# Optimization experiments

Measured on AMD Instinct MI355X. Metric: run time of the kernel, lower is better.

The kernel has to match this reference:

```python
import jax, jax.numpy as jnp
import numpy as np
from jax.scipy.linalg import expm

LATENT, HIDDEN, N_PARTS, K = 128, 2048, 128, 2048
OMEGA_DIM, TRANZ_DIM = 9 * N_PARTS, 3 * N_PARTS


def setup_inputs() -> dict:
    key = jax.random.key(0)
    ks = jax.random.split(key, 10)

    def w(k, out_d, in_d):
        # eqx.nn.Linear-style scale ~ 1/sqrt(fan_in)
        return jax.random.normal(k, (out_d, in_d), dtype=jnp.float32) / np.sqrt(in_d)

    return {
        "x_init": jax.random.normal(ks[0], (LATENT, K), dtype=jnp.float32),
        "Wo0": w(ks[1], HIDDEN, LATENT),
        "Wo1": w(ks[2], HIDDEN, HIDDEN),
        "Wo2": w(ks[3], HIDDEN, HIDDEN),
        "Wo3": w(ks[4], OMEGA_DIM, HIDDEN),
        "Wt0": w(ks[5], HIDDEN, LATENT),
        "Wt1": w(ks[6], HIDDEN, HIDDEN),
        "Wt2": w(ks[7], HIDDEN, HIDDEN),
        "Wt3": w(ks[8], TRANZ_DIM, HIDDEN),
    }


def _mlp(weights, x):
    # bias-free MLP, relu on all but last layer; x is (d_in, K)
    for i, W in enumerate(weights):
        x = W @ x
        if i + 1 < len(weights):
            x = jax.nn.relu(x)
    return x


def reference(x_init, Wo0, Wo1, Wo2, Wo3, Wt0, Wt1, Wt2, Wt3):
    omega = _mlp([Wo0, Wo1, Wo2, Wo3], x_init)            # (9n, K)
    n = omega.shape[0] // 9
    k = omega.shape[1]
    # exp_omega 2D branch: vmap over columns, each column -> (n,3,3) expm batch
    mats = omega.T.reshape(k * n, 3, 3)
    R = jax.vmap(expm)(mats).reshape(k, 9 * n)            # (K, 9n)
    rotations = R.T                                        # (9n, K)
    translations = _mlp([Wt0, Wt1, Wt2, Wt3], x_init)     # (3n, K)
    # form_transformations (2D branch): stack translation as a 4th row -> (12n, K)
    rot_r = rotations.reshape(n, 3, 3, k)
    tr_r = translations.reshape(n, 1, 3, k)
    transf = jnp.concatenate([rot_r, tr_r], axis=1).reshape(-1, k)  # (12n, K)
    return (omega, transf, rotations, translations)
```

## Files before the change

kernel.cpp:

```cpp
#include <hip/hip_runtime.h>
#include <stdint.h>


typedef short bf16x8 __attribute__((ext_vector_type(8)));
typedef float f32x4 __attribute__((ext_vector_type(4)));

__device__ __forceinline__ unsigned short f2bf(float f) {
  unsigned int x = __float_as_uint(f);
  unsigned int r = (x + 0x7fffu + ((x >> 16) & 1u)) >> 16;
  return (unsigned short)r;
}

__device__ __forceinline__ void gld_lds16(const void* g, void* l) {
  __builtin_amdgcn_global_load_lds(
      (__attribute__((address_space(1))) void*)(g),
      (__attribute__((address_space(3))) void*)(l),
      16, 0, 0);
}

__global__ void cast_weights_k(const float* __restrict__ wo0, const float* __restrict__ wo1,
                               const float* __restrict__ wo2, const float* __restrict__ wo3,
                               const float* __restrict__ wt0, const float* __restrict__ wt1,
                               const float* __restrict__ wt2, const float* __restrict__ wt3,
                               unsigned short* __restrict__ dst) {
  int gid = blockIdx.x * 256 + threadIdx.x;
  int idx = gid * 4;
  if (idx >= 20447232) return;
  const float* src;
  int off;
  if (idx < 8650752) {
    if (idx < 262144)       { src = wo0; off = idx; }
    else if (idx < 4456448) { src = wo1; off = idx - 262144; }
    else                    { src = wo2; off = idx - 4456448; }
  } else {
    if (idx < 11010048)      { src = wo3; off = idx - 8650752; }
    else if (idx < 11272192) { src = wt0; off = idx - 11010048; }
    else if (idx < 15466496) { src = wt1; off = idx - 11272192; }
    else if (idx < 19660800) { src = wt2; off = idx - 15466496; }
    else                     { src = wt3; off = idx - 19660800; }
  }
  float4 v = *(const float4*)(src + off);
  ushort4 o;
  o.x = f2bf(v.x); o.y = f2bf(v.y); o.z = f2bf(v.z); o.w = f2bf(v.w);
  *(ushort4*)(dst + idx) = o;
}

__global__ void transpose_cast_k(const float* __restrict__ x, unsigned short* __restrict__ xt) {
  __shared__ float tile[32][33];
  const int bx = blockIdx.x, by = blockIdx.y;
  const int tx = threadIdx.x, ty = threadIdx.y;
#pragma unroll
  for (int i = 0; i < 32; i += 8)
    tile[ty + i][tx] = x[(size_t)(by * 32 + ty + i) * 2048 + bx * 32 + tx];
  __syncthreads();
#pragma unroll
  for (int i = 0; i < 32; i += 8)
    xt[(size_t)(bx * 32 + ty + i) * 128 + by * 32 + tx] = f2bf(tile[tx][ty + i]);
}

template <int MODE, int TM, int SWZ>
__global__ __launch_bounds__(256, 2) void gemm_tn(
    const unsigned short* __restrict__ A0, const unsigned short* __restrict__ B0,
    void* __restrict__ C0v, int n0tiles, int ldc0, long csplit0,
    const unsigned short* __restrict__ A1, const unsigned short* __restrict__ B1,
    void* __restrict__ C1v, int ldc1, long csplit1, int Kfull, int Klen) {
  __shared__ unsigned short Asl[TM * 64];
  __shared__ unsigned short Bsl[128 * 64];
  constexpr int TMW = TM / 32;

  int mt, yt;
  if (SWZ) {
    int id = blockIdx.x;
    int xcd = id & 7, s = id >> 3;
    mt = ((xcd & 1) << 3) + (s & 7);
    yt = ((xcd >> 1) << 3) + (s >> 3);
  } else {
    mt = blockIdx.x;
    yt = blockIdx.y;
  }

  const unsigned short* A;
  const unsigned short* B;
  char* C;
  int ldc;
  long csplit;
  if (yt < n0tiles) { A = A0; B = B0; C = (char*)C0v; ldc = ldc0; csplit = csplit0; }
  else { A = A1; B = B1; C = (char*)C1v; ldc = ldc1; csplit = csplit1; yt -= n0tiles; }
  C += (long)blockIdx.z * csplit;

  const int k0base = blockIdx.z * Klen;
  const unsigned short* Ab = A + (size_t)mt * TM * Kfull;
  const unsigned short* Bb = B + (size_t)yt * 128 * Kfull;

  const int tid = threadIdx.x;
  const int wave = tid >> 6, lane = tid & 63;
  const int mw = (wave >> 1) * (TM / 2), nw = (wave & 1) * 64;
  const int l16 = lane & 15, quad = lane >> 4;

  f32x4 acc[TMW][4] = {};

  for (int k0 = k0base; k0 < k0base + Klen; k0 += 64) {
#pragma unroll
    for (int i = 0; i < TM / 32; ++i) {
      int c = i * 256 + tid;
      int row = c >> 3;
      int sseg = (c & 7) ^ (row & 7);
      gld_lds16(Ab + (size_t)row * Kfull + k0 + sseg * 8, &Asl[c * 8]);
    }
#pragma unroll
    for (int i = 0; i < 4; ++i) {
      int c = i * 256 + tid;
      int row = c >> 3;
      int sseg = (c & 7) ^ (row & 7);
      gld_lds16(Bb + (size_t)row * Kfull + k0 + sseg * 8, &Bsl[c * 8]);
    }
    __syncthreads();

#pragma unroll
    for (int h = 0; h < 2; ++h) {
      bf16x8 af[TMW], bfr[4];
#pragma unroll
      for (int t = 0; t < TMW; ++t) {
        int row = mw + t * 16 + l16;
        int p = (h * 4 + quad) ^ (row & 7);
        af[t] = *(const bf16x8*)&Asl[row * 64 + p * 8];
      }
#pragma unroll
      for (int t = 0; t < 4; ++t) {
        int row = nw + t * 16 + l16;
        int p = (h * 4 + quad) ^ (row & 7);
        bfr[t] = *(const bf16x8*)&Bsl[row * 64 + p * 8];
      }
#pragma unroll
      for (int tm = 0; tm < TMW; ++tm)
#pragma unroll
        for (int tn = 0; tn < 4; ++tn)
          acc[tm][tn] = __builtin_amdgcn_mfma_f32_16x16x32_bf16(af[tm], bfr[tn], acc[tm][tn], 0, 0, 0);
    }
    __syncthreads();
  }

  const int mbase = mt * TM + mw;
  const int nbase = yt * 128 + nw;
#pragma unroll
  for (int tm = 0; tm < TMW; ++tm) {
#pragma unroll
    for (int tn = 0; tn < 4; ++tn) {
      int col = nbase + tn * 16 + l16;
      int row0 = mbase + tm * 16 + quad * 4;
#pragma unroll
      for (int r = 0; r < 4; ++r) {
        float v = acc[tm][tn][r];
        if (MODE == 0) {
          v = fmaxf(v, 0.0f);
          ((unsigned short*)C)[(size_t)(row0 + r) * ldc + col] = f2bf(v);
        } else {
          ((float*)C)[(size_t)(row0 + r) * ldc + col] = v;
        }
      }
    }
  }
}

__device__ __forceinline__ void mm3(const float* a, const float* b, float* c) {
#pragma unroll
  for (int r = 0; r < 3; ++r)
#pragma unroll
    for (int cc = 0; cc < 3; ++cc)
      c[r * 3 + cc] = a[r * 3 + 0] * b[0 + cc] + a[r * 3 + 1] * b[3 + cc] + a[r * 3 + 2] * b[6 + cc];
}

__global__ void finalize_k(const float* __restrict__ om_p, const float* __restrict__ tr_p,
                           float* __restrict__ out) {
  const int k = blockIdx.x * 256 + threadIdx.x;
  const int j = blockIdx.y;

  float a[9];
#pragma unroll
  for (int i = 0; i < 9; ++i)
    a[i] = om_p[(size_t)k * 1152 + 9 * j + i] + om_p[2359296 + (size_t)k * 1152 + 9 * j + i];

  float* omega  = out;
  float* transf = out + (size_t)1152 * 2048;
  float* rot    = out + (size_t)(1152 + 1536) * 2048;
  float* transl = out + (size_t)(1152 + 1536 + 1152) * 2048;

#pragma unroll
  for (int i = 0; i < 9; ++i) omega[(size_t)(9 * j + i) * 2048 + k] = a[i];

  float n1 = 0.f;
#pragma unroll
  for (int c = 0; c < 3; ++c) {
    float s = fabsf(a[c]) + fabsf(a[3 + c]) + fabsf(a[6 + c]);
    n1 = fmaxf(n1, s);
  }
  int s = 0;
  if (n1 > 0.25f) {
    s = (int)ceilf(log2f(n1 * 4.0f));
    if (s < 0) s = 0;
  }
  const float scl = exp2f((float)(-s));
  float As[9];
#pragma unroll
  for (int i = 0; i < 9; ++i) As[i] = a[i] * scl;

  float E[9] = {1, 0, 0, 0, 1, 0, 0, 0, 1};
  float T[9] = {1, 0, 0, 0, 1, 0, 0, 0, 1};
#pragma unroll
  for (int t = 1; t <= 12; ++t) {
    float Tn[9];
    mm3(T, As, Tn);
    const float inv = 1.0f / (float)t;
#pragma unroll
    for (int i = 0; i < 9; ++i) { T[i] = Tn[i] * inv; E[i] += T[i]; }
  }
  for (int q = 0; q < s; ++q) {
    float Tn[9];
    mm3(E, E, Tn);
#pragma unroll
    for (int i = 0; i < 9; ++i) E[i] = Tn[i];
  }

#pragma unroll
  for (int i = 0; i < 9; ++i) {
    rot[(size_t)(9 * j + i) * 2048 + k] = E[i];
    transf[(size_t)(12 * j + i) * 2048 + k] = E[i];
  }
  float tr[3];
#pragma unroll
  for (int c = 0; c < 3; ++c)
    tr[c] = tr_p[(size_t)k * 384 + 3 * j + c] + tr_p[786432 + (size_t)k * 384 + 3 * j + c];
#pragma unroll
  for (int c = 0; c < 3; ++c) {
    transf[(size_t)(12 * j + 9 + c) * 2048 + k] = tr[c];
    transl[(size_t)(3 * j + c) * 2048 + k] = tr[c];
  }
}

extern "C" void kernel_launch(void* const* d_in, const int* in_sizes, int n_in,
                              void* d_out, int out_size, void* d_ws, size_t ws_size,
                              hipStream_t stream) {
  const float* x   = (const float*)d_in[0];
  const float* Wo0 = (const float*)d_in[1];
  const float* Wo1 = (const float*)d_in[2];
  const float* Wo2 = (const float*)d_in[3];
  const float* Wo3 = (const float*)d_in[4];
  const float* Wt0 = (const float*)d_in[5];
  const float* Wt1 = (const float*)d_in[6];
  const float* Wt2 = (const float*)d_in[7];
  const float* Wt3 = (const float*)d_in[8];

  unsigned short* wb   = (unsigned short*)d_ws;
  unsigned short* wo0b = wb + 0;
  unsigned short* wo1b = wb + 262144;
  unsigned short* wo2b = wb + 4456448;
  unsigned short* wo3b = wb + 8650752;
  unsigned short* wt0b = wb + 11010048;
  unsigned short* wt1b = wb + 11272192;
  unsigned short* wt2b = wb + 15466496;
  unsigned short* wt3b = wb + 19660800;
  unsigned short* Xt   = wb + 20447232;
  unsigned short* HoA  = Xt + 262144;
  unsigned short* HoB  = HoA + 4194304;
  unsigned short* HtA  = HoB + 4194304;
  unsigned short* HtB  = HtA + 4194304;
  float* om_p = (float*)(HtB + 4194304);
  float* tr_p = om_p + 2 * 2359296;

  cast_weights_k<<<19968, 256, 0, stream>>>(Wo0, Wo1, Wo2, Wo3, Wt0, Wt1, Wt2, Wt3, wb);
  transpose_cast_k<<<dim3(64, 4), dim3(32, 8), 0, stream>>>(x, Xt);

  gemm_tn<0, 128, 1><<<512, 256, 0, stream>>>(Xt, wo0b, HoA, 16, 2048, 0,
                                              Xt, wt0b, HtA, 2048, 0, 128, 128);
  gemm_tn<0, 128, 1><<<512, 256, 0, stream>>>(HoA, wo1b, HoB, 16, 2048, 0,
                                              HtA, wt1b, HtB, 2048, 0, 2048, 2048);
  gemm_tn<0, 128, 1><<<512, 256, 0, stream>>>(HoB, wo2b, HoA, 16, 2048, 0,
                                              HtB, wt2b, HtA, 2048, 0, 2048, 2048);
  gemm_tn<1, 64, 0><<<dim3(32, 12, 2), 256, 0, stream>>>(
      HoA, wo3b, om_p, 9, 1152, (long)2359296 * 4,
      HtA, wt3b, tr_p, 384, (long)786432 * 4, 2048, 1024);

  finalize_k<<<dim3(8, 128), 256, 0, stream>>>(om_p, tr_p, (float*)d_out);
}
```

Measured before the change: 258.1 us.

## Double GEMM K-step to 128, transpose partial outputs, widen weight cast

The GEMM mainloop now stages 128-wide K slices in LDS with a 16-way XOR swizzle, halving the number of barrier-separated iterations. The final-layer GEMM writes its fp32 partials transposed with 16-byte vector stores, so the finalize kernel reads them coalesced along k. The weight cast kernel processes 8 elements per thread. The larger LDS footprint may reduce occupancy or raise register pressure.

```diff
diff --git a/kernel.cpp b/kernel.cpp
--- a/kernel.cpp
+++ b/kernel.cpp
@@ -24,7 +24,7 @@
                                const float* __restrict__ wt2, const float* __restrict__ wt3,
                                unsigned short* __restrict__ dst) {
   int gid = blockIdx.x * 256 + threadIdx.x;
-  int idx = gid * 4;
+  int idx = gid * 8;
   if (idx >= 20447232) return;
   const float* src;
   int off;
@@ -39,10 +39,14 @@
     else if (idx < 19660800) { src = wt2; off = idx - 15466496; }
     else                     { src = wt3; off = idx - 19660800; }
   }
-  float4 v = *(const float4*)(src + off);
-  ushort4 o;
-  o.x = f2bf(v.x); o.y = f2bf(v.y); o.z = f2bf(v.z); o.w = f2bf(v.w);
-  *(ushort4*)(dst + idx) = o;
+  float4 a = *(const float4*)(src + off);
+  float4 b = *(const float4*)(src + off + 4);
+  uint4 o;
+  o.x = (unsigned)f2bf(a.x) | ((unsigned)f2bf(a.y) << 16);
+  o.y = (unsigned)f2bf(a.z) | ((unsigned)f2bf(a.w) << 16);
+  o.z = (unsigned)f2bf(b.x) | ((unsigned)f2bf(b.y) << 16);
+  o.w = (unsigned)f2bf(b.z) | ((unsigned)f2bf(b.w) << 16);
+  *(uint4*)(dst + idx) = o;
 }
 
 __global__ void transpose_cast_k(const float* __restrict__ x, unsigned short* __restrict__ xt) {
@@ -64,8 +68,8 @@
     void* __restrict__ C0v, int n0tiles, int ldc0, long csplit0,
     const unsigned short* __restrict__ A1, const unsigned short* __restrict__ B1,
     void* __restrict__ C1v, int ldc1, long csplit1, int Kfull, int Klen) {
-  __shared__ unsigned short Asl[TM * 64];
-  __shared__ unsigned short Bsl[128 * 64];
+  __shared__ alignas(16) unsigned short Asl[TM * 128];
+  __shared__ alignas(16) unsigned short Bsl[128 * 128];
   constexpr int TMW = TM / 32;
 
   int mt, yt;
@@ -99,37 +103,37 @@
 
   f32x4 acc[TMW][4] = {};
 
-  for (int k0 = k0base; k0 < k0base + Klen; k0 += 64) {
-#pragma unroll
-    for (int i = 0; i < TM / 32; ++i) {
+  for (int k0 = k0base; k0 < k0base + Klen; k0 += 128) {
+#pragma unroll
+    for (int i = 0; i < TM / 16; ++i) {
       int c = i * 256 + tid;
-      int row = c >> 3;
-      int sseg = (c & 7) ^ (row & 7);
-      gld_lds16(Ab + (size_t)row * Kfull + k0 + sseg * 8, &Asl[c * 8]);
-    }
-#pragma unroll
-    for (int i = 0; i < 4; ++i) {
+      int row = c >> 4;
+      int l = (c & 15) ^ (row & 15);
+      gld_lds16(Ab + (size_t)row * Kfull + k0 + l * 8, &Asl[c * 8]);
+    }
+#pragma unroll
+    for (int i = 0; i < 8; ++i) {
       int c = i * 256 + tid;
-      int row = c >> 3;
-      int sseg = (c & 7) ^ (row & 7);
-      gld_lds16(Bb + (size_t)row * Kfull + k0 + sseg * 8, &Bsl[c * 8]);
+      int row = c >> 4;
+      int l = (c & 15) ^ (row & 15);
+      gld_lds16(Bb + (size_t)row * Kfull + k0 + l * 8, &Bsl[c * 8]);
     }
     __syncthreads();
 
 #pragma unroll
-    for (int h = 0; h < 2; ++h) {
+    for (int h = 0; h < 4; ++h) {
       bf16x8 af[TMW], bfr[4];
 #pragma unroll
       for (int t = 0; t < TMW; ++t) {
         int row = mw + t * 16 + l16;
-        int p = (h * 4 + quad) ^ (row & 7);
-        af[t] = *(const bf16x8*)&Asl[row * 64 + p * 8];
+        int p = (h * 4 + quad) ^ (row & 15);
+        af[t] = *(const bf16x8*)&Asl[row * 128 + p * 8];
       }
 #pragma unroll
       for (int t = 0; t < 4; ++t) {
         int row = nw + t * 16 + l16;
-        int p = (h * 4 + quad) ^ (row & 7);
-        bfr[t] = *(const bf16x8*)&Bsl[row * 64 + p * 8];
+        int p = (h * 4 + quad) ^ (row & 15);
+        bfr[t] = *(const bf16x8*)&Bsl[row * 128 + p * 8];
       }
 #pragma unroll
       for (int tm = 0; tm < TMW; ++tm)
@@ -148,15 +152,14 @@
     for (int tn = 0; tn < 4; ++tn) {
       int col = nbase + tn * 16 + l16;
       int row0 = mbase + tm * 16 + quad * 4;
-#pragma unroll
-      for (int r = 0; r < 4; ++r) {
-        float v = acc[tm][tn][r];
-        if (MODE == 0) {
-          v = fmaxf(v, 0.0f);
+      if (MODE == 0) {
+#pragma unroll
+        for (int r = 0; r < 4; ++r) {
+          float v = fmaxf(acc[tm][tn][r], 0.0f);
           ((unsigned short*)C)[(size_t)(row0 + r) * ldc + col] = f2bf(v);
-        } else {
-          ((float*)C)[(size_t)(row0 + r) * ldc + col] = v;
         }
+      } else {
+        *(f32x4*)((float*)C + (size_t)col * ldc + row0) = acc[tm][tn];
       }
     }
   }
@@ -178,7 +181,7 @@
   float a[9];
 #pragma unroll
   for (int i = 0; i < 9; ++i)
-    a[i] = om_p[(size_t)k * 1152 + 9 * j + i] + om_p[2359296 + (size_t)k * 1152 + 9 * j + i];
+    a[i] = om_p[(size_t)(9 * j + i) * 2048 + k] + om_p[2359296 + (size_t)(9 * j + i) * 2048 + k];
 
   float* omega  = out;
   float* transf = out + (size_t)1152 * 2048;
@@ -229,7 +232,7 @@
   float tr[3];
 #pragma unroll
   for (int c = 0; c < 3; ++c)
-    tr[c] = tr_p[(size_t)k * 384 + 3 * j + c] + tr_p[786432 + (size_t)k * 384 + 3 * j + c];
+    tr[c] = tr_p[(size_t)(3 * j + c) * 2048 + k] + tr_p[786432 + (size_t)(3 * j + c) * 2048 + k];
 #pragma unroll
   for (int c = 0; c < 3; ++c) {
     transf[(size_t)(12 * j + 9 + c) * 2048 + k] = tr[c];
@@ -267,7 +270,7 @@
   float* om_p = (float*)(HtB + 4194304);
   float* tr_p = om_p + 2 * 2359296;
 
-  cast_weights_k<<<19968, 256, 0, stream>>>(Wo0, Wo1, Wo2, Wo3, Wt0, Wt1, Wt2, Wt3, wb);
+  cast_weights_k<<<9984, 256, 0, stream>>>(Wo0, Wo1, Wo2, Wo3, Wt0, Wt1, Wt2, Wt3, wb);
   transpose_cast_k<<<dim3(64, 4), dim3(32, 8), 0, stream>>>(x, Xt);
 
   gemm_tn<0, 128, 1><<<512, 256, 0, stream>>>(Xt, wo0b, HoA, 16, 2048, 0,
@@ -277,8 +280,8 @@
   gemm_tn<0, 128, 1><<<512, 256, 0, stream>>>(HoB, wo2b, HoA, 16, 2048, 0,
                                               HtB, wt2b, HtA, 2048, 0, 2048, 2048);
   gemm_tn<1, 64, 0><<<dim3(32, 12, 2), 256, 0, stream>>>(
-      HoA, wo3b, om_p, 9, 1152, (long)2359296 * 4,
-      HtA, wt3b, tr_p, 384, (long)786432 * 4, 2048, 1024);
+      HoA, wo3b, om_p, 9, 2048, (long)2359296 * 4,
+      HtA, wt3b, tr_p, 2048, (long)786432 * 4, 2048, 1024);
 
   finalize_k<<<dim3(8, 128), 256, 0, stream>>>(om_p, tr_p, (float*)d_out);
 }
```

After: 246.1 us. -4.7%, faster.
